# Performance work log

Measured on AMD Instinct MI355X. Metric: run time of the kernel, lower is better.

## Reference

```python
import jax, jax.numpy as jnp
import numpy as np

EMBED = 1024
HEADS = 16
HEAD_DIM = EMBED // HEADS


def setup_inputs() -> dict:
    key = jax.random.key(0)
    ks = jax.random.split(key, 9)
    B, S = 2, 2048
    values = jax.random.normal(ks[0], (B, S, EMBED), dtype=jnp.float32)
    keys_in = jax.random.normal(ks[1], (B, S, EMBED), dtype=jnp.float32)
    query = jax.random.normal(ks[2], (B, S, EMBED), dtype=jnp.float32)
    mask = jax.random.randint(ks[3], (B, 1, 1, S), 0, 2, dtype=jnp.int32)
    # torch Linear weights: [out_features, in_features], y = x @ W.T
    sc = 1.0 / np.sqrt(HEAD_DIM)
    Wv = jax.random.uniform(ks[4], (HEAD_DIM, HEAD_DIM), jnp.float32, -sc, sc)
    Wk = jax.random.uniform(ks[5], (HEAD_DIM, HEAD_DIM), jnp.float32, -sc, sc)
    Wq = jax.random.uniform(ks[6], (HEAD_DIM, HEAD_DIM), jnp.float32, -sc, sc)
    so = 1.0 / np.sqrt(EMBED)
    Wo = jax.random.uniform(ks[7], (EMBED, EMBED), jnp.float32, -so, so)
    bo = jax.random.uniform(ks[8], (EMBED,), jnp.float32, -so, so)
    return {"values": values, "keys": keys_in, "query": query, "mask": mask,
            "Wv": Wv, "Wk": Wk, "Wq": Wq, "Wo": Wo, "bo": bo}


def reference(values, keys, query, mask, Wv, Wk, Wq, Wo, bo):
    B = query.shape[0]
    # split heads: [B, S, H, D]
    v = values.reshape(B, -1, HEADS, HEAD_DIM)
    k = keys.reshape(B, -1, HEADS, HEAD_DIM)
    q = query.reshape(B, -1, HEADS, HEAD_DIM)
    # per-head shared linear projections (nn.Linear on last dim, no bias)
    v = jnp.einsum('bshd,ed->bshe', v, Wv)
    k = jnp.einsum('bshd,ed->bshe', k, Wk)
    q = jnp.einsum('bshd,ed->bshe', q, Wq)
    # energy: [B, H, Q, K]
    energy = jnp.einsum('bqhd,bkhd->bhqk', q, k)
    energy = jnp.where(mask == 0, jnp.float32(-1e20), energy)
    attn = jax.nn.softmax(energy / jnp.sqrt(jnp.float32(EMBED)), axis=3)
    out = jnp.einsum('bhqk,bkhd->bqhd', attn, v).reshape(B, -1, EMBED)
    return out @ Wo.T + bo
```

## Files before the change

kernel.cpp:

```cpp
#include <hip/hip_runtime.h>
#include <hip/hip_bf16.h>


typedef __attribute__((ext_vector_type(8))) short bf16x8;
typedef __attribute__((ext_vector_type(4))) float f32x4;
typedef __attribute__((ext_vector_type(16))) float f32x16;
typedef __attribute__((ext_vector_type(2))) int i32x2;

__device__ int g_srcidx[2 * 2048];
__device__ int g_NK[2];

__device__ __forceinline__ short f2bf(float x) {
  union { float f; unsigned u; } v; v.f = x;
  unsigned r = v.u + 0x7FFFu + ((v.u >> 16) & 1u);
  return (short)(r >> 16);
}

__device__ __forceinline__ int pack2(float lo, float hi) {
  __hip_bfloat162 h = __float22bfloat162_rn(make_float2(lo, hi));
  int r; __builtin_memcpy(&r, &h, 4); return r;
}

__device__ __forceinline__ bf16x8 cvt8(float4 a, float4 b) {
  union { int i[4]; bf16x8 h; } u;
  u.i[0] = pack2(a.x, a.y);
  u.i[1] = pack2(a.z, a.w);
  u.i[2] = pack2(b.x, b.y);
  u.i[3] = pack2(b.z, b.w);
  return u.h;
}

__device__ __forceinline__ void plsw(int& a, int& b) {
  i32x2 r = __builtin_amdgcn_permlane32_swap(a, b, false, false);
  a = r[0]; b = r[1];
}
__device__ __forceinline__ float pl_comb_add(float v) {
  int a = __float_as_int(v), b = a;
  i32x2 r = __builtin_amdgcn_permlane32_swap(a, b, false, false);
  return __int_as_float(r[0]) + __int_as_float(r[1]);
}

__device__ __forceinline__ void gll16(const short* g, short* l) {
  __builtin_amdgcn_global_load_lds(
      (const __attribute__((address_space(1))) void*)g,
      (__attribute__((address_space(3))) void*)l, 16, 0, 0);
}

__global__ __launch_bounds__(256) void prep_kernel(const int* __restrict__ mask) {
  __shared__ int cnt[256];
  const int t = threadIdx.x;
  const int b = blockIdx.x;
  const int* m = mask + b * 2048;
  int* sidx = g_srcidx + b * 2048;
  const int base = t * 8;
  int vals[8], lc = 0;
#pragma unroll
  for (int i = 0; i < 8; i++) { vals[i] = (m[base + i] != 0); lc += vals[i]; }
  cnt[t] = lc;
  __syncthreads();
  for (int off = 1; off < 256; off <<= 1) {
    int v = (t >= off) ? cnt[t - off] : 0;
    __syncthreads();
    cnt[t] += v;
    __syncthreads();
  }
  int pos = cnt[t] - lc;
  const int total = cnt[255];
#pragma unroll
  for (int i = 0; i < 8; i++)
    if (vals[i]) sidx[pos++] = base + i;
  for (int j = total + t; j < 2048; j += 256) sidx[j] = 0;
  if (t == 0) g_NK[b] = total;
}

__global__ __launch_bounds__(256) void proj_kernel(
    const float* __restrict__ keys, const float* __restrict__ query,
    const float* __restrict__ values,
    const float* __restrict__ Wk, const float* __restrict__ Wq,
    const float* __restrict__ Wv, const float* __restrict__ Wo,
    short* __restrict__ Kp, short* __restrict__ Qp, short* __restrict__ Vt,
    short* __restrict__ WoB) {
  const int bid0 = blockIdx.x;
  const int t = threadIdx.x;
  if (bid0 >= 3072) {
    int i = ((bid0 - 3072) * 256 + t) * 8;
    float4 a = *(const float4*)(Wo + i), b2 = *(const float4*)(Wo + i + 4);
    *(bf16x8*)(WoB + i) = cvt8(a, b2);
    return;
  }
  const int w = t >> 6, l = t & 63, l15 = l & 15, l4 = l >> 4;
  __shared__ short Al[64 * 64];
  __shared__ short Bl[64 * 64];
  __shared__ short Tl[64 * 66];

  if (bid0 < 2048) {
    int bid = bid0;
    const float* X = keys; const float* W = Wk; short* O = Kp;
    bool isq = false;
    if (bid >= 1024) { X = query; W = Wq; O = Qp; bid -= 1024; isq = true; }
    const int r0 = bid << 6;
    const int bb = r0 >> 15;
    if (!isq) {
      const int j0 = (r0 >> 4) & 2047;
      const int jlim = (g_NK[bb] + 63) & ~63;
      if (j0 >= jlim) return;
    }
#pragma unroll
    for (int i = 0; i < 2; i++) {
      int c = t + (i << 8);
      int row = c >> 3, col8 = c & 7;
      int pc = col8 ^ (row & 7);
      int ri = r0 + row;
      int j = (ri >> 4) & 2047, hh = ri & 15;
      int s = isq ? j : g_srcidx[(bb << 11) + j];
      const float* xs = X + ((size_t)((bb * 2048 + s) * 16 + hh)) * 64 + col8 * 8;
      float4 a0 = *(const float4*)xs, a1 = *(const float4*)(xs + 4);
      *(bf16x8*)&Al[row * 64 + pc * 8] = cvt8(a0, a1);
      const float* wsrc = W + row * 64 + col8 * 8;
      float4 b0 = *(const float4*)wsrc, b1 = *(const float4*)(wsrc + 4);
      *(bf16x8*)&Bl[row * 64 + pc * 8] = cvt8(b0, b1);
    }
    __syncthreads();
    f32x4 acc[4];
#pragma unroll
    for (int i = 0; i < 4; i++) acc[i] = (f32x4){0.f, 0.f, 0.f, 0.f};
#pragma unroll
    for (int kc = 0; kc < 2; kc++) {
      int ar = w * 16 + l15;
      bf16x8 af = *(const bf16x8*)((const char*)Al +
          ((ar * 128 + kc * 64 + l4 * 16) ^ ((ar & 7) << 4)));
#pragma unroll
      for (int ng = 0; ng < 4; ng++) {
        int br = ng * 16 + l15;
        bf16x8 bfr = *(const bf16x8*)((const char*)Bl +
            ((br * 128 + kc * 64 + l4 * 16) ^ ((br & 7) << 4)));
        acc[ng] = __builtin_amdgcn_mfma_f32_16x16x32_bf16(af, bfr, acc[ng], 0, 0, 0);
      }
    }
    const float osc = isq ? (1.4426950408889634f / 32.0f) : 1.0f;
#pragma unroll
    for (int ng = 0; ng < 4; ng++) {
#pragma unroll
      for (int j = 0; j < 4; j++) {
        int ri = r0 + w * 16 + l4 * 4 + j;
        int e = ng * 16 + l15;
        int b2 = ri >> 15, jj = (ri >> 4) & 2047, hh = ri & 15;
        O[(((size_t)(b2 * 16 + hh)) * 2048 + jj) * 64 + e] = f2bf(acc[ng][j] * osc);
      }
    }
  } else {
    const int bid = bid0 - 2048;
    const int st = bid & 31, bh = bid >> 5;
    const int b = bh >> 4, h = bh & 15;
    const int s0 = st << 6;
    const int jlim = (g_NK[b] + 63) & ~63;
    if (s0 >= jlim) return;
#pragma unroll
    for (int i = 0; i < 2; i++) {
      int c = t + (i << 8);
      int row = c >> 3, col8 = c & 7;
      int pc = col8 ^ (row & 7);
      int s = g_srcidx[(b << 11) + s0 + row];
      const float* xs = values + ((size_t)(b * 2048 + s)) * 1024 + h * 64 + col8 * 8;
      float4 a0 = *(const float4*)xs, a1 = *(const float4*)(xs + 4);
      *(bf16x8*)&Al[row * 64 + pc * 8] = cvt8(a0, a1);
      const float* wsrc = Wv + row * 64 + col8 * 8;
      float4 b0 = *(const float4*)wsrc, b1 = *(const float4*)(wsrc + 4);
      *(bf16x8*)&Bl[row * 64 + pc * 8] = cvt8(b0, b1);
    }
    __syncthreads();
    f32x4 acc[4];
#pragma unroll
    for (int i = 0; i < 4; i++) acc[i] = (f32x4){0.f, 0.f, 0.f, 0.f};
#pragma unroll
    for (int kc = 0; kc < 2; kc++) {
      int ar = w * 16 + l15;
      bf16x8 af = *(const bf16x8*)((const char*)Al +
          ((ar * 128 + kc * 64 + l4 * 16) ^ ((ar & 7) << 4)));
#pragma unroll
      for (int ng = 0; ng < 4; ng++) {
        int br = ng * 16 + l15;
        bf16x8 bfr = *(const bf16x8*)((const char*)Bl +
            ((br * 128 + kc * 64 + l4 * 16) ^ ((br & 7) << 4)));
        acc[ng] = __builtin_amdgcn_mfma_f32_16x16x32_bf16(af, bfr, acc[ng], 0, 0, 0);
      }
    }
#pragma unroll
    for (int ng = 0; ng < 4; ng++) {
#pragma unroll
      for (int j = 0; j < 4; j++) {
        Tl[(w * 16 + l4 * 4 + j) * 66 + ng * 16 + l15] = f2bf(acc[ng][j]);
      }
    }
    __syncthreads();
    int e = t >> 2, sc = (t & 3) << 4;
    bf16x8 o0, o1;
#pragma unroll
    for (int i = 0; i < 8; i++) {
      o0[i] = Tl[(sc + i) * 66 + e];
      o1[i] = Tl[(sc + 8 + i) * 66 + e];
    }
    short* dst = Vt + ((size_t)bh * 64 + e) * 2048 + s0 + sc;
    *(bf16x8*)dst = o0;
    *(bf16x8*)(dst + 8) = o1;
  }
}

__global__ __launch_bounds__(256, 2) void attn_kernel(
    const short* __restrict__ Qp, const short* __restrict__ Kp,
    const short* __restrict__ Vt, short* __restrict__ AO) {
  const int bid = (int)(blockIdx.x % 8) * 64 + (int)(blockIdx.x / 8);
  const int qb = bid & 15, bh = bid >> 4;
  const int b = bh >> 4, h = bh & 15;
  const int t = threadIdx.x;
  const int w = t >> 6, l = t & 63, l31 = l & 31, hi = l >> 5;
  const int q0w = qb * 128 + w * 32;

  __shared__ short Kl[2][64 * 64];
  __shared__ short Vl[2][64 * 64];
  __shared__ float Cl[4 * 32];

  const short* Kbase = Kp + (size_t)bh * 2048 * 64;
  const short* Vbase = Vt + (size_t)bh * 64 * 2048;

  const int nk = g_NK[b];
  const int ntiles = (nk + 63) >> 6;

  const short* qptr = Qp + ((size_t)bh * 2048 + q0w + l31) * 64 + hi * 8;
  bf16x8 qf[4];
#pragma unroll
  for (int dc = 0; dc < 4; dc++) qf[dc] = *(const bf16x8*)(qptr + dc * 16);

  int laddr[2][4];
#pragma unroll
  for (int x = 0; x < 2; x++) {
    int rr = x * 32 + l31;
#pragma unroll
    for (int c2 = 0; c2 < 4; c2++)
      laddr[x][c2] = rr * 128 + (((c2 * 32) + hi * 16) ^ ((rr & 7) << 4));
  }

  const int srow = t >> 3, scol = t & 7;
  const int sc0 = (scol ^ (srow & 7)) * 8;
  const short* ksrc0 = Kbase + srow * 64 + sc0;
  const short* ksrc1 = Kbase + (srow + 32) * 64 + sc0;
  const short* vsrc0 = Vbase + (size_t)srow * 2048 + sc0;
  const short* vsrc1 = Vbase + (size_t)(srow + 32) * 2048 + sc0;
  short* klds = &Kl[0][0];
  short* vlds = &Vl[0][0];
  const int d0 = t * 8, d1 = t * 8 + 2048;

  gll16(ksrc0, klds + d0);
  gll16(ksrc1, klds + d1);
  gll16(vsrc0, vlds + d0);
  gll16(vsrc1, vlds + d1);
  __syncthreads();

  float l_run = 0.f;
  f32x16 o0, o1;
#pragma unroll
  for (int r = 0; r < 16; r++) { o0[r] = 0.f; o1[r] = 0.f; }

  for (int kt = 0; kt < ntiles; kt++) {
    const int bs = kt & 1;
    const int bsb = bs << 13;
    if (kt + 1 < ntiles) {
      const int nb = (bs ^ 1) << 12;
      gll16(ksrc0 + (kt + 1) * 4096, klds + nb + d0);
      gll16(ksrc1 + (kt + 1) * 4096, klds + nb + d1);
      gll16(vsrc0 + (kt + 1) * 64, vlds + nb + d0);
      gll16(vsrc1 + (kt + 1) * 64, vlds + nb + d1);
    }

    f32x16 st0, st1;
#pragma unroll
    for (int r = 0; r < 16; r++) { st0[r] = 0.f; st1[r] = 0.f; }
    __builtin_amdgcn_s_setprio(1);
#pragma unroll
    for (int dc = 0; dc < 4; dc++) {
      bf16x8 ka = *(const bf16x8*)((const char*)Kl + bsb + laddr[0][dc]);
      st0 = __builtin_amdgcn_mfma_f32_32x32x16_bf16(ka, qf[dc], st0, 0, 0, 0);
    }
#pragma unroll
    for (int dc = 0; dc < 4; dc++) {
      bf16x8 kb = *(const bf16x8*)((const char*)Kl + bsb + laddr[1][dc]);
      st1 = __builtin_amdgcn_mfma_f32_32x32x16_bf16(kb, qf[dc], st1, 0, 0, 0);
    }
    __builtin_amdgcn_s_setprio(0);

    if (((kt << 6) + 64) <= nk) {
#pragma unroll
      for (int r = 0; r < 16; r++) {
        st0[r] = __builtin_amdgcn_exp2f(st0[r]);
        st1[r] = __builtin_amdgcn_exp2f(st1[r]);
      }
    } else {
      const int kb2 = kt << 6;
#pragma unroll
      for (int r = 0; r < 16; r++) {
        int cr = (r & 3) + 8 * (r >> 2) + 4 * hi;
        float e0 = __builtin_amdgcn_exp2f(st0[r]);
        float e1 = __builtin_amdgcn_exp2f(st1[r]);
        st0[r] = (kb2 + cr < nk) ? e0 : 0.f;
        st1[r] = (kb2 + 32 + cr < nk) ? e1 : 0.f;
      }
    }

    float sx[8];
#pragma unroll
    for (int i = 0; i < 8; i++)
      sx[i] = (st0[2 * i] + st0[2 * i + 1]) + (st1[2 * i] + st1[2 * i + 1]);
#pragma unroll
    for (int s2 = 4; s2 > 0; s2 >>= 1)
#pragma unroll
      for (int i = 0; i < 4; i++)
        if (i < s2) sx[i] += sx[i + s2];
    l_run += pl_comb_add(sx[0]);

    bf16x8 pa[4];
#pragma unroll
    for (int kc = 0; kc < 4; kc++) {
      int bse = (kc & 1) * 8;
      float p0, p1, p2, p3, p4, p5, p6, p7;
      if (kc < 2) {
        p0 = st0[bse + 0]; p1 = st0[bse + 1]; p2 = st0[bse + 2]; p3 = st0[bse + 3];
        p4 = st0[bse + 4]; p5 = st0[bse + 5]; p6 = st0[bse + 6]; p7 = st0[bse + 7];
      } else {
        p0 = st1[bse + 0]; p1 = st1[bse + 1]; p2 = st1[bse + 2]; p3 = st1[bse + 3];
        p4 = st1[bse + 4]; p5 = st1[bse + 5]; p6 = st1[bse + 6]; p7 = st1[bse + 7];
      }
      int A0 = pack2(p0, p1), A1 = pack2(p2, p3);
      int B0 = pack2(p4, p5), B1 = pack2(p6, p7);
      plsw(A0, B0);
      plsw(A1, B1);
      union { int4 i; bf16x8 h; } u;
      u.i = make_int4(A0, A1, B0, B1);
      pa[kc] = u.h;
    }

    __builtin_amdgcn_s_setprio(1);
#pragma unroll
    for (int kc = 0; kc < 4; kc++) {
      bf16x8 vf = *(const bf16x8*)((const char*)Vl + bsb + laddr[0][kc]);
      o0 = __builtin_amdgcn_mfma_f32_32x32x16_bf16(pa[kc], vf, o0, 0, 0, 0);
    }
#pragma unroll
    for (int kc = 0; kc < 4; kc++) {
      bf16x8 vf = *(const bf16x8*)((const char*)Vl + bsb + laddr[1][kc]);
      o1 = __builtin_amdgcn_mfma_f32_32x32x16_bf16(pa[kc], vf, o1, 0, 0, 0);
    }
    __builtin_amdgcn_s_setprio(0);
    __syncthreads();
  }

  float invr = 1.0f / l_run;
  Cl[w * 32 + l31] = invr;
  short* aob = AO + ((size_t)(b * 2048 + q0w)) * 1024 + h * 64 + l31;
#pragma unroll
  for (int r = 0; r < 16; r++) {
    int qr = (r & 3) + 8 * (r >> 2) + 4 * hi;
    float ic = Cl[w * 32 + qr];
    aob[(size_t)qr * 1024] = f2bf(o0[r] * ic);
    aob[(size_t)qr * 1024 + 32] = f2bf(o1[r] * ic);
  }
}

__global__ __launch_bounds__(512) void outproj_kernel(
    const short* __restrict__ AO, const short* __restrict__ WoB,
    const float* __restrict__ bo, float* __restrict__ Cout) {
  const int bid = (int)(blockIdx.x % 8) * 32 + (int)(blockIdx.x / 8);
  const int mt = bid >> 3, nt = bid & 7;
  const int m0 = mt << 7, n0 = nt << 7;
  const int t = threadIdx.x;
  const int w = t >> 6, wr = w >> 2, wc = w & 3;
  const int l = t & 63, l15 = l & 15, l4 = l >> 4;
  __shared__ short Al[2][128 * 64];
  __shared__ short Bl[2][128 * 64];

  const short* asrc[2];
  const short* bsrc[2];
  int ldst[2];
#pragma unroll
  for (int i = 0; i < 2; i++) {
    int c = t + (i << 9);
    int row = c >> 3, col8 = c & 7;
    int sc = (col8 ^ (row & 7)) * 8;
    asrc[i] = AO + (size_t)(m0 + row) * 1024 + sc;
    bsrc[i] = WoB + (size_t)(n0 + row) * 1024 + sc;
    ldst[i] = c * 8;
  }
  short* al = &Al[0][0];
  short* bl = &Bl[0][0];

  auto stage = [&](int ks, int bs) {
    const int nb = bs << 13;
    const int ko = ks * 64;
#pragma unroll
    for (int i = 0; i < 2; i++) {
      gll16(asrc[i] + ko, al + nb + ldst[i]);
      gll16(bsrc[i] + ko, bl + nb + ldst[i]);
    }
  };

  stage(0, 0);
  __syncthreads();

  f32x4 acc[4][2];
#pragma unroll
  for (int mi = 0; mi < 4; mi++)
#pragma unroll
    for (int ni = 0; ni < 2; ni++) acc[mi][ni] = (f32x4){0.f, 0.f, 0.f, 0.f};

  for (int ks = 0; ks < 16; ks++) {
    const int bs = ks & 1, bsb = bs << 14;
    if (ks < 15) stage(ks + 1, bs ^ 1);
#pragma unroll
    for (int kc = 0; kc < 2; kc++) {
      bf16x8 af[4];
#pragma unroll
      for (int mi = 0; mi < 4; mi++) {
        int ar = wr * 64 + mi * 16 + l15;
        af[mi] = *(const bf16x8*)((const char*)Al + bsb +
            ((ar * 128 + kc * 64 + l4 * 16) ^ ((ar & 7) << 4)));
      }
#pragma unroll
      for (int ni = 0; ni < 2; ni++) {
        int br = wc * 32 + ni * 16 + l15;
        bf16x8 bfr = *(const bf16x8*)((const char*)Bl + bsb +
            ((br * 128 + kc * 64 + l4 * 16) ^ ((br & 7) << 4)));
#pragma unroll
        for (int mi = 0; mi < 4; mi++)
          acc[mi][ni] = __builtin_amdgcn_mfma_f32_16x16x32_bf16(
              af[mi], bfr, acc[mi][ni], 0, 0, 0);
      }
    }
    __syncthreads();
  }

#pragma unroll
  for (int ni = 0; ni < 2; ni++) {
    int n = n0 + wc * 32 + ni * 16 + l15;
    float bias = bo[n];
#pragma unroll
    for (int mi = 0; mi < 4; mi++) {
#pragma unroll
      for (int j = 0; j < 4; j++) {
        int m = m0 + wr * 64 + mi * 16 + l4 * 4 + j;
        Cout[(size_t)m * 1024 + n] = acc[mi][ni][j] + bias;
      }
    }
  }
}

extern "C" void kernel_launch(void* const* d_in, const int* in_sizes, int n_in,
                              void* d_out, int out_size, void* d_ws, size_t ws_size,
                              hipStream_t stream) {
  const float* values = (const float*)d_in[0];
  const float* keys   = (const float*)d_in[1];
  const float* query  = (const float*)d_in[2];
  const int*   mask   = (const int*)d_in[3];
  const float* Wv = (const float*)d_in[4];
  const float* Wk = (const float*)d_in[5];
  const float* Wq = (const float*)d_in[6];
  const float* Wo = (const float*)d_in[7];
  const float* bo = (const float*)d_in[8];
  float* out = (float*)d_out;
  char* ws = (char*)d_ws;
  short* Qp  = (short*)(ws + (size_t)0);
  short* Kp  = (short*)(ws + ((size_t)8 << 20));
  short* Vtp = (short*)(ws + ((size_t)16 << 20));
  short* AO  = (short*)(ws + ((size_t)24 << 20));
  short* WoB = (short*)(ws + ((size_t)32 << 20));

  prep_kernel<<<2, 256, 0, stream>>>(mask);
  proj_kernel<<<3584, 256, 0, stream>>>(keys, query, values, Wk, Wq, Wv, Wo,
                                        Kp, Qp, Vtp, WoB);
  attn_kernel<<<512, 256, 0, stream>>>(Qp, Kp, Vtp, AO);
  outproj_kernel<<<256, 512, 0, stream>>>(AO, WoB, bo, out);
}
```

Before: 65.39 us.

## Fuse Q projection into attention kernel prologue

Moves the per-head Q projection out of the projection kernel and into the attention kernel. Each attention wave loads its raw fp32 query rows, multiplies them by Wq with MFMA, applies the softmax scale, and stages the result through shared memory into the Q fragments. This removes the 1024 Q-projection blocks and the bf16 Qp write and read round trip to global memory. In exchange, the attention prologue gains extra global loads, MFMA work and two barriers.

```diff
diff --git a/kernel.cpp b/kernel.cpp
--- a/kernel.cpp
+++ b/kernel.cpp
@@ -74,16 +74,14 @@
 }
 
 __global__ __launch_bounds__(256) void proj_kernel(
-    const float* __restrict__ keys, const float* __restrict__ query,
-    const float* __restrict__ values,
-    const float* __restrict__ Wk, const float* __restrict__ Wq,
-    const float* __restrict__ Wv, const float* __restrict__ Wo,
-    short* __restrict__ Kp, short* __restrict__ Qp, short* __restrict__ Vt,
-    short* __restrict__ WoB) {
+    const float* __restrict__ keys, const float* __restrict__ values,
+    const float* __restrict__ Wk, const float* __restrict__ Wv,
+    const float* __restrict__ Wo,
+    short* __restrict__ Kp, short* __restrict__ Vt, short* __restrict__ WoB) {
   const int bid0 = blockIdx.x;
   const int t = threadIdx.x;
-  if (bid0 >= 3072) {
-    int i = ((bid0 - 3072) * 256 + t) * 8;
+  if (bid0 >= 2048) {
+    int i = ((bid0 - 2048) * 256 + t) * 8;
     float4 a = *(const float4*)(Wo + i), b2 = *(const float4*)(Wo + i + 4);
     *(bf16x8*)(WoB + i) = cvt8(a, b2);
     return;
@@ -93,18 +91,12 @@
   __shared__ short Bl[64 * 64];
   __shared__ short Tl[64 * 66];
 
-  if (bid0 < 2048) {
-    int bid = bid0;
-    const float* X = keys; const float* W = Wk; short* O = Kp;
-    bool isq = false;
-    if (bid >= 1024) { X = query; W = Wq; O = Qp; bid -= 1024; isq = true; }
-    const int r0 = bid << 6;
+  if (bid0 < 1024) {
+    const int r0 = bid0 << 6;
     const int bb = r0 >> 15;
-    if (!isq) {
-      const int j0 = (r0 >> 4) & 2047;
-      const int jlim = (g_NK[bb] + 63) & ~63;
-      if (j0 >= jlim) return;
-    }
+    const int j0 = (r0 >> 4) & 2047;
+    const int jlim = (g_NK[bb] + 63) & ~63;
+    if (j0 >= jlim) return;
 #pragma unroll
     for (int i = 0; i < 2; i++) {
       int c = t + (i << 8);
@@ -112,11 +104,11 @@
       int pc = col8 ^ (row & 7);
       int ri = r0 + row;
       int j = (ri >> 4) & 2047, hh = ri & 15;
-      int s = isq ? j : g_srcidx[(bb << 11) + j];
-      const float* xs = X + ((size_t)((bb * 2048 + s) * 16 + hh)) * 64 + col8 * 8;
+      int s = g_srcidx[(bb << 11) + j];
+      const float* xs = keys + ((size_t)((bb * 2048 + s) * 16 + hh)) * 64 + col8 * 8;
       float4 a0 = *(const float4*)xs, a1 = *(const float4*)(xs + 4);
       *(bf16x8*)&Al[row * 64 + pc * 8] = cvt8(a0, a1);
-      const float* wsrc = W + row * 64 + col8 * 8;
+      const float* wsrc = Wk + row * 64 + col8 * 8;
       float4 b0 = *(const float4*)wsrc, b1 = *(const float4*)(wsrc + 4);
       *(bf16x8*)&Bl[row * 64 + pc * 8] = cvt8(b0, b1);
     }
@@ -137,7 +129,6 @@
         acc[ng] = __builtin_amdgcn_mfma_f32_16x16x32_bf16(af, bfr, acc[ng], 0, 0, 0);
       }
     }
-    const float osc = isq ? (1.4426950408889634f / 32.0f) : 1.0f;
 #pragma unroll
     for (int ng = 0; ng < 4; ng++) {
 #pragma unroll
@@ -145,11 +136,11 @@
         int ri = r0 + w * 16 + l4 * 4 + j;
         int e = ng * 16 + l15;
         int b2 = ri >> 15, jj = (ri >> 4) & 2047, hh = ri & 15;
-        O[(((size_t)(b2 * 16 + hh)) * 2048 + jj) * 64 + e] = f2bf(acc[ng][j] * osc);
+        Kp[(((size_t)(b2 * 16 + hh)) * 2048 + jj) * 64 + e] = f2bf(acc[ng][j]);
       }
     }
   } else {
-    const int bid = bid0 - 2048;
+    const int bid = bid0 - 1024;
     const int st = bid & 31, bh = bid >> 5;
     const int b = bh >> 4, h = bh & 15;
     const int s0 = st << 6;
@@ -207,8 +198,9 @@
 }
 
 __global__ __launch_bounds__(256, 2) void attn_kernel(
-    const short* __restrict__ Qp, const short* __restrict__ Kp,
-    const short* __restrict__ Vt, short* __restrict__ AO) {
+    const float* __restrict__ query, const float* __restrict__ Wq,
+    const short* __restrict__ Kp, const short* __restrict__ Vt,
+    short* __restrict__ AO) {
   const int bid = (int)(blockIdx.x % 8) * 64 + (int)(blockIdx.x / 8);
   const int qb = bid & 15, bh = bid >> 4;
   const int b = bh >> 4, h = bh & 15;
@@ -226,10 +218,49 @@
   const int nk = g_NK[b];
   const int ntiles = (nk + 63) >> 6;
 
-  const short* qptr = Qp + ((size_t)bh * 2048 + q0w + l31) * 64 + hi * 8;
+  const float SC2 = 1.4426950408889634f / 32.0f;
+  {
+    const float* qsrc = query + ((size_t)(b * 2048 + q0w + l31)) * 1024 +
+                        h * 64 + hi * 8;
+    f32x16 qc0, qc1;
+#pragma unroll
+    for (int r = 0; r < 16; r++) { qc0[r] = 0.f; qc1[r] = 0.f; }
+#pragma unroll
+    for (int ec = 0; ec < 4; ec++) {
+      float4 xq0 = *(const float4*)(qsrc + ec * 16);
+      float4 xq1 = *(const float4*)(qsrc + ec * 16 + 4);
+      bf16x8 bq = cvt8(xq0, xq1);
+      const float* w0 = Wq + (size_t)l31 * 64 + ec * 16 + hi * 8;
+      bf16x8 aw0 = cvt8(*(const float4*)w0, *(const float4*)(w0 + 4));
+      qc0 = __builtin_amdgcn_mfma_f32_32x32x16_bf16(aw0, bq, qc0, 0, 0, 0);
+      const float* w1 = Wq + (size_t)(32 + l31) * 64 + ec * 16 + hi * 8;
+      bf16x8 aw1 = cvt8(*(const float4*)w1, *(const float4*)(w1 + 4));
+      qc1 = __builtin_amdgcn_mfma_f32_32x32x16_bf16(aw1, bq, qc1, 0, 0, 0);
+    }
+    short* Ql = &Kl[0][0];
+    const int qrow = w * 32 + l31;
+#pragma unroll
+    for (int i = 0; i < 8; i++) {
+      int p0 = pack2(qc0[2 * i] * SC2, qc0[2 * i + 1] * SC2);
+      int p1 = pack2(qc1[2 * i] * SC2, qc1[2 * i + 1] * SC2);
+      int d0 = (i >> 1) * 8 + (i & 1) * 2 + 4 * hi;
+      int off0 = (qrow * 128 + d0 * 2) ^ ((qrow & 7) << 4);
+      int off1 = (qrow * 128 + (32 + d0) * 2) ^ ((qrow & 7) << 4);
+      *(int*)((char*)Ql + off0) = p0;
+      *(int*)((char*)Ql + off1) = p1;
+    }
+  }
+  __syncthreads();
   bf16x8 qf[4];
-#pragma unroll
-  for (int dc = 0; dc < 4; dc++) qf[dc] = *(const bf16x8*)(qptr + dc * 16);
+  {
+    const short* Ql = &Kl[0][0];
+    const int rrq = w * 32 + l31;
+#pragma unroll
+    for (int dc = 0; dc < 4; dc++)
+      qf[dc] = *(const bf16x8*)((const char*)Ql +
+          ((rrq * 128 + dc * 32 + hi * 16) ^ ((rrq & 7) << 4)));
+  }
+  __syncthreads();
 
   int laddr[2][4];
 #pragma unroll
@@ -466,15 +497,13 @@
   const float* bo = (const float*)d_in[8];
   float* out = (float*)d_out;
   char* ws = (char*)d_ws;
-  short* Qp  = (short*)(ws + (size_t)0);
   short* Kp  = (short*)(ws + ((size_t)8 << 20));
   short* Vtp = (short*)(ws + ((size_t)16 << 20));
   short* AO  = (short*)(ws + ((size_t)24 << 20));
   short* WoB = (short*)(ws + ((size_t)32 << 20));
 
   prep_kernel<<<2, 256, 0, stream>>>(mask);
-  proj_kernel<<<3584, 256, 0, stream>>>(keys, query, values, Wk, Wq, Wv, Wo,
-                                        Kp, Qp, Vtp, WoB);
-  attn_kernel<<<512, 256, 0, stream>>>(Qp, Kp, Vtp, AO);
+  proj_kernel<<<2560, 256, 0, stream>>>(keys, values, Wk, Wv, Wo, Kp, Vtp, WoB);
+  attn_kernel<<<512, 256, 0, stream>>>(query, Wq, Kp, Vtp, AO);
   outproj_kernel<<<256, 512, 0, stream>>>(AO, WoB, bo, out);
 }
```

New measurement: 67.22 us. +2.8%, slower.

## Load K/V fragments directly into registers and move Wo conversion into attention launch

Applied to the files above, without the earlier changes.

The attention kernel stops staging K and V tiles through double-buffered shared memory with async global-to-LDS copies. Each lane now reads its MFMA fragments straight from global memory into registers, using a two-stage register ping-pong so the next tile's loads are issued before the current tile is computed, and the per-tile __syncthreads goes away. The Wo-to-bf16 conversion blocks move from the projection launch to extra blocks in the attention launch. The cost is redundant global/L2 reads, since waves sharing the same K/V no longer share an LDS copy, plus much higher register pressure from the buffered fragments.

```diff
diff --git a/kernel.cpp b/kernel.cpp
--- a/kernel.cpp
+++ b/kernel.cpp
@@ -77,17 +77,10 @@
     const float* __restrict__ keys, const float* __restrict__ query,
     const float* __restrict__ values,
     const float* __restrict__ Wk, const float* __restrict__ Wq,
-    const float* __restrict__ Wv, const float* __restrict__ Wo,
-    short* __restrict__ Kp, short* __restrict__ Qp, short* __restrict__ Vt,
-    short* __restrict__ WoB) {
+    const float* __restrict__ Wv,
+    short* __restrict__ Kp, short* __restrict__ Qp, short* __restrict__ Vt) {
   const int bid0 = blockIdx.x;
   const int t = threadIdx.x;
-  if (bid0 >= 3072) {
-    int i = ((bid0 - 3072) * 256 + t) * 8;
-    float4 a = *(const float4*)(Wo + i), b2 = *(const float4*)(Wo + i + 4);
-    *(bf16x8*)(WoB + i) = cvt8(a, b2);
-    return;
-  }
   const int w = t >> 6, l = t & 63, l15 = l & 15, l4 = l >> 4;
   __shared__ short Al[64 * 64];
   __shared__ short Bl[64 * 64];
@@ -208,7 +201,14 @@
 
 __global__ __launch_bounds__(256, 2) void attn_kernel(
     const short* __restrict__ Qp, const short* __restrict__ Kp,
-    const short* __restrict__ Vt, short* __restrict__ AO) {
+    const short* __restrict__ Vt, short* __restrict__ AO,
+    const float* __restrict__ Wo, short* __restrict__ WoB) {
+  if (blockIdx.x >= 512) {
+    int i = (((int)blockIdx.x - 512) * 256 + (int)threadIdx.x) * 8;
+    float4 a = *(const float4*)(Wo + i), b2 = *(const float4*)(Wo + i + 4);
+    *(bf16x8*)(WoB + i) = cvt8(a, b2);
+    return;
+  }
   const int bid = (int)(blockIdx.x % 8) * 64 + (int)(blockIdx.x / 8);
   const int qb = bid & 15, bh = bid >> 4;
   const int b = bh >> 4, h = bh & 15;
@@ -216,8 +216,6 @@
   const int w = t >> 6, l = t & 63, l31 = l & 31, hi = l >> 5;
   const int q0w = qb * 128 + w * 32;
 
-  __shared__ short Kl[2][64 * 64];
-  __shared__ short Vl[2][64 * 64];
   __shared__ float Cl[4 * 32];
 
   const short* Kbase = Kp + (size_t)bh * 2048 * 64;
@@ -231,61 +229,48 @@
 #pragma unroll
   for (int dc = 0; dc < 4; dc++) qf[dc] = *(const bf16x8*)(qptr + dc * 16);
 
-  int laddr[2][4];
-#pragma unroll
-  for (int x = 0; x < 2; x++) {
-    int rr = x * 32 + l31;
-#pragma unroll
-    for (int c2 = 0; c2 < 4; c2++)
-      laddr[x][c2] = rr * 128 + (((c2 * 32) + hi * 16) ^ ((rr & 7) << 4));
-  }
-
-  const int srow = t >> 3, scol = t & 7;
-  const int sc0 = (scol ^ (srow & 7)) * 8;
-  const short* ksrc0 = Kbase + srow * 64 + sc0;
-  const short* ksrc1 = Kbase + (srow + 32) * 64 + sc0;
-  const short* vsrc0 = Vbase + (size_t)srow * 2048 + sc0;
-  const short* vsrc1 = Vbase + (size_t)(srow + 32) * 2048 + sc0;
-  short* klds = &Kl[0][0];
-  short* vlds = &Vl[0][0];
-  const int d0 = t * 8, d1 = t * 8 + 2048;
-
-  gll16(ksrc0, klds + d0);
-  gll16(ksrc1, klds + d1);
-  gll16(vsrc0, vlds + d0);
-  gll16(vsrc1, vlds + d1);
-  __syncthreads();
+  const short* kb[2] = { Kbase + (size_t)l31 * 64 + hi * 8,
+                         Kbase + (size_t)(32 + l31) * 64 + hi * 8 };
+  const short* vb[2] = { Vbase + (size_t)l31 * 2048 + hi * 8,
+                         Vbase + (size_t)(32 + l31) * 2048 + hi * 8 };
 
   float l_run = 0.f;
   f32x16 o0, o1;
 #pragma unroll
   for (int r = 0; r < 16; r++) { o0[r] = 0.f; o1[r] = 0.f; }
 
-  for (int kt = 0; kt < ntiles; kt++) {
-    const int bs = kt & 1;
-    const int bsb = bs << 13;
-    if (kt + 1 < ntiles) {
-      const int nb = (bs ^ 1) << 12;
-      gll16(ksrc0 + (kt + 1) * 4096, klds + nb + d0);
-      gll16(ksrc1 + (kt + 1) * 4096, klds + nb + d1);
-      gll16(vsrc0 + (kt + 1) * 64, vlds + nb + d0);
-      gll16(vsrc1 + (kt + 1) * 64, vlds + nb + d1);
-    }
-
+  bf16x8 kfA[2][4], vfA[2][4], kfB[2][4], vfB[2][4];
+
+  auto loadA = [&](int kt) {
+#pragma unroll
+    for (int x = 0; x < 2; x++)
+#pragma unroll
+      for (int c = 0; c < 4; c++) {
+        kfA[x][c] = *(const bf16x8*)(kb[x] + (size_t)kt * 4096 + c * 16);
+        vfA[x][c] = *(const bf16x8*)(vb[x] + kt * 64 + c * 16);
+      }
+  };
+  auto loadB = [&](int kt) {
+#pragma unroll
+    for (int x = 0; x < 2; x++)
+#pragma unroll
+      for (int c = 0; c < 4; c++) {
+        kfB[x][c] = *(const bf16x8*)(kb[x] + (size_t)kt * 4096 + c * 16);
+        vfB[x][c] = *(const bf16x8*)(vb[x] + kt * 64 + c * 16);
+      }
+  };
+
+  auto compute = [&](int kt, bf16x8 (&kf)[2][4], bf16x8 (&vf)[2][4]) {
     f32x16 st0, st1;
 #pragma unroll
     for (int r = 0; r < 16; r++) { st0[r] = 0.f; st1[r] = 0.f; }
     __builtin_amdgcn_s_setprio(1);
 #pragma unroll
-    for (int dc = 0; dc < 4; dc++) {
-      bf16x8 ka = *(const bf16x8*)((const char*)Kl + bsb + laddr[0][dc]);
-      st0 = __builtin_amdgcn_mfma_f32_32x32x16_bf16(ka, qf[dc], st0, 0, 0, 0);
-    }
-#pragma unroll
-    for (int dc = 0; dc < 4; dc++) {
-      bf16x8 kb = *(const bf16x8*)((const char*)Kl + bsb + laddr[1][dc]);
-      st1 = __builtin_amdgcn_mfma_f32_32x32x16_bf16(kb, qf[dc], st1, 0, 0, 0);
-    }
+    for (int dc = 0; dc < 4; dc++)
+      st0 = __builtin_amdgcn_mfma_f32_32x32x16_bf16(kf[0][dc], qf[dc], st0, 0, 0, 0);
+#pragma unroll
+    for (int dc = 0; dc < 4; dc++)
+      st1 = __builtin_amdgcn_mfma_f32_32x32x16_bf16(kf[1][dc], qf[dc], st1, 0, 0, 0);
     __builtin_amdgcn_s_setprio(0);
 
     if (((kt << 6) + 64) <= nk) {
@@ -340,17 +325,22 @@
 
     __builtin_amdgcn_s_setprio(1);
 #pragma unroll
-    for (int kc = 0; kc < 4; kc++) {
-      bf16x8 vf = *(const bf16x8*)((const char*)Vl + bsb + laddr[0][kc]);
-      o0 = __builtin_amdgcn_mfma_f32_32x32x16_bf16(pa[kc], vf, o0, 0, 0, 0);
-    }
-#pragma unroll
-    for (int kc = 0; kc < 4; kc++) {
-      bf16x8 vf = *(const bf16x8*)((const char*)Vl + bsb + laddr[1][kc]);
-      o1 = __builtin_amdgcn_mfma_f32_32x32x16_bf16(pa[kc], vf, o1, 0, 0, 0);
-    }
+    for (int kc = 0; kc < 4; kc++)
+      o0 = __builtin_amdgcn_mfma_f32_32x32x16_bf16(pa[kc], vf[0][kc], o0, 0, 0, 0);
+#pragma unroll
+    for (int kc = 0; kc < 4; kc++)
+      o1 = __builtin_amdgcn_mfma_f32_32x32x16_bf16(pa[kc], vf[1][kc], o1, 0, 0, 0);
     __builtin_amdgcn_s_setprio(0);
-    __syncthreads();
+  };
+
+  loadA(0);
+  for (int kt = 0; kt < ntiles; kt += 2) {
+    if (kt + 1 < ntiles) loadB(kt + 1);
+    compute(kt, kfA, vfA);
+    if (kt + 1 < ntiles) {
+      if (kt + 2 < ntiles) loadA(kt + 2);
+      compute(kt + 1, kfB, vfB);
+    }
   }
 
   float invr = 1.0f / l_run;
@@ -473,8 +463,8 @@
   short* WoB = (short*)(ws + ((size_t)32 << 20));
 
   prep_kernel<<<2, 256, 0, stream>>>(mask);
-  proj_kernel<<<3584, 256, 0, stream>>>(keys, query, values, Wk, Wq, Wv, Wo,
-                                        Kp, Qp, Vtp, WoB);
-  attn_kernel<<<512, 256, 0, stream>>>(Qp, Kp, Vtp, AO);
+  proj_kernel<<<3072, 256, 0, stream>>>(keys, query, values, Wk, Wq, Wv,
+                                        Kp, Qp, Vtp);
+  attn_kernel<<<1024, 256, 0, stream>>>(Qp, Kp, Vtp, AO, Wo, WoB);
   outproj_kernel<<<256, 512, 0, stream>>>(AO, WoB, bo, out);
 }
```

Result: slower. 101.4 us (+55.1%).
